# Optimization experiments

Hardware: AMD Instinct MI355X
Metric: run time of the kernel (lower is better)

Reference implementation:

```python
import jax, jax.numpy as jnp
import numpy as np

D = 768      # model dim
H = 12       # heads
HD = D // H  # head dim
FF = 3072    # mlp hidden = 4*D
EPS = 1e-5   # torch LayerNorm default eps


def setup_inputs() -> dict:
    key = jax.random.key(0)
    ks = jax.random.split(key, 8)
    init = lambda k, shp: (jax.random.normal(k, shp, jnp.float32) * 0.02)
    return {
        "x1": jax.random.normal(ks[0], (8, 512, D), jnp.float32),
        "x2": jax.random.normal(ks[1], (8, 1024, D), jnp.float32),
        "ln1_g": jnp.ones((D,), jnp.float32),
        "ln1_b": jnp.zeros((D,), jnp.float32),
        "w_qkv": init(ks[2], (D, 3 * D)),
        "b_qkv": jnp.zeros((3 * D,), jnp.float32),
        "w_proj": init(ks[3], (D, D)),
        "b_proj": jnp.zeros((D,), jnp.float32),
        "ls1": jnp.full((D,), 1e-5, jnp.float32),
        "ln2_g": jnp.ones((D,), jnp.float32),
        "ln2_b": jnp.zeros((D,), jnp.float32),
        "w_fc1": init(ks[4], (D, FF)),
        "b_fc1": jnp.zeros((FF,), jnp.float32),
        "w_fc2": init(ks[5], (FF, D)),
        "b_fc2": jnp.zeros((D,), jnp.float32),
        "ls2": jnp.full((D,), 1e-5, jnp.float32),
    }


def _ln(x, g, b):
    m = x.mean(-1, keepdims=True)
    v = ((x - m) ** 2).mean(-1, keepdims=True)
    return (x - m) * jax.lax.rsqrt(v + EPS) * g + b


def _block(x, ln1_g, ln1_b, w_qkv, b_qkv, w_proj, b_proj, ls1,
           ln2_g, ln2_b, w_fc1, b_fc1, w_fc2, b_fc2, ls2):
    # Block-diagonal attention over same-length group == independent per-sequence MHA.
    b, n, _ = x.shape
    h = _ln(x, ln1_g, ln1_b)
    qkv = h @ w_qkv + b_qkv                       # [b, n, 3D]
    q, k, v = [t.reshape(b, n, H, HD).transpose(0, 2, 1, 3)
               for t in jnp.split(qkv, 3, axis=-1)]
    scores = jnp.einsum('bhqd,bhkd->bhqk', q, k) * (HD ** -0.5)
    attn = jax.nn.softmax(scores, axis=-1)
    o = jnp.einsum('bhqk,bhkd->bhqd', attn, v).transpose(0, 2, 1, 3).reshape(b, n, D)
    x = x + ls1 * (o @ w_proj + b_proj)           # LayerScale + residual
    h2 = _ln(x, ln2_g, ln2_b)
    mlp = jax.nn.gelu(h2 @ w_fc1 + b_fc1, approximate=False) @ w_fc2 + b_fc2
    return x + ls2 * mlp


def reference(x1, x2, ln1_g, ln1_b, w_qkv, b_qkv, w_proj, b_proj, ls1,
              ln2_g, ln2_b, w_fc1, b_fc1, w_fc2, b_fc2, ls2):
    params = (ln1_g, ln1_b, w_qkv, b_qkv, w_proj, b_proj, ls1,
              ln2_g, ln2_b, w_fc1, b_fc1, w_fc2, b_fc2, ls2)
    y1 = _block(x1, *params)
    y2 = _block(x2, *params)
    # concatenated varlen token stream, equivalent to pre-split cat tensor
    return jnp.concatenate([y1.reshape(-1, D), y2.reshape(-1, D)], axis=0)
```

## Files before the change

### kernel.cpp

```cpp
#include <hip/hip_runtime.h>
#include <hip/hip_bf16.h>
#include <math.h>

typedef __hip_bfloat16 bf16_t;
typedef __bf16 bf16x8 __attribute__((ext_vector_type(8)));
typedef float f32x4 __attribute__((ext_vector_type(4)));
typedef float f32x16 __attribute__((ext_vector_type(16)));
typedef int int32x8 __attribute__((ext_vector_type(8)));
typedef int int4v __attribute__((ext_vector_type(4)));
typedef short short8v __attribute__((ext_vector_type(8)));

__device__ __forceinline__ void load_lds16(const void* g, void* l) {
    __builtin_amdgcn_global_load_lds(
        (__attribute__((address_space(1))) void*)g,
        (__attribute__((address_space(3))) void*)l, 16, 0, 0);
}

__device__ __forceinline__ unsigned char f32_fp8(float x) {
    return (unsigned char)(__builtin_amdgcn_cvt_pk_fp8_f32(x, 0.f, 0, false) & 0xff);
}

__global__ __launch_bounds__(256) void wconv_kernel(
    const float* __restrict__ W, unsigned char* __restrict__ Wt, int K, int N)
{
    __shared__ float tile[32][33];
    const int k0 = blockIdx.x * 32, n0 = blockIdx.y * 32;
    const int tx = threadIdx.x & 31, ty = threadIdx.x >> 5;
    #pragma unroll
    for (int i = 0; i < 32; i += 8)
        tile[ty + i][tx] = W[(size_t)(k0 + ty + i) * N + n0 + tx];
    __syncthreads();
    #pragma unroll
    for (int i = 0; i < 32; i += 8)
        Wt[(size_t)(n0 + ty + i) * K + k0 + tx] = f32_fp8(tile[tx][ty + i] * 64.f);
}

__global__ __launch_bounds__(256) void ln_kernel(
    const float* __restrict__ x0, const float* __restrict__ x1, int split,
    const float* __restrict__ g, const float* __restrict__ b,
    unsigned char* __restrict__ out)
{
    const int t = blockIdx.x;
    const int tid = threadIdx.x;
    const float* xr = (t < split) ? x0 + (size_t)t * 768
                                  : x1 + (size_t)(t - split) * 768;
    float v[3], s = 0.f, q = 0.f;
    #pragma unroll
    for (int i = 0; i < 3; ++i) {
        v[i] = xr[tid + i * 256];
        s += v[i]; q += v[i] * v[i];
    }
    #pragma unroll
    for (int o = 32; o > 0; o >>= 1) {
        s += __shfl_down(s, o);
        q += __shfl_down(q, o);
    }
    __shared__ float rs_[4], rq_[4];
    const int w = tid >> 6, lane = tid & 63;
    if (lane == 0) { rs_[w] = s; rq_[w] = q; }
    __syncthreads();
    s = rs_[0] + rs_[1] + rs_[2] + rs_[3];
    q = rq_[0] + rq_[1] + rq_[2] + rq_[3];
    const float mean = s * (1.f / 768.f);
    const float var  = q * (1.f / 768.f) - mean * mean;
    const float rstd = rsqrtf(var + 1e-5f);
    unsigned char* orow = out + (size_t)t * 768;
    #pragma unroll
    for (int i = 0; i < 3; ++i) {
        const int d = tid + i * 256;
        orow[d] = f32_fp8((v[i] - mean) * rstd * g[d] + b[d]);
    }
}

__device__ __forceinline__ int32x8 frag32(const unsigned char* S, int row, int lh) {
    const int rot = (row >> 1) & 3;
    const int t0 = lh * 2;
    const int4v lo = *(const int4v*)&S[row * 64 + (((t0 + rot) & 3) << 4)];
    const int4v hi = *(const int4v*)&S[row * 64 + (((t0 + 1 + rot) & 3) << 4)];
    int32x8 r;
    r[0] = lo[0]; r[1] = lo[1]; r[2] = lo[2]; r[3] = lo[3];
    r[4] = hi[0]; r[5] = hi[1]; r[6] = hi[2]; r[7] = hi[3];
    return r;
}

__global__ __launch_bounds__(256) void gemm_kernel(
    const unsigned char* __restrict__ A, const unsigned char* __restrict__ Bt,
    const float* __restrict__ bias, const float* __restrict__ ls,
    const float* __restrict__ resid0, const float* __restrict__ resid1, int rsplit,
    void* __restrict__ outp, bf16_t* __restrict__ vtout,
    int M, int N, int K, int mode)
{
    __shared__ __align__(16) unsigned char As[128 * 64];
    __shared__ __align__(16) unsigned char Bs[128 * 64];
    const int tid  = threadIdx.x;
    const int lane = tid & 63;
    const int w    = tid >> 6;
    const int wm   = w >> 1, wn = w & 1;
    const int l32  = lane & 31, lh = lane >> 5;
    const int bm   = blockIdx.x, bn = blockIdx.y;

    f32x16 acc[2][2];
    #pragma unroll
    for (int i = 0; i < 2; ++i)
        #pragma unroll
        for (int j = 0; j < 2; ++j)
            #pragma unroll
            for (int e = 0; e < 16; ++e) acc[i][j][e] = 0.f;

    const int srow   = lane >> 2;
    const int schunk = lane & 3;
    const unsigned char* Ag = A  + (size_t)(bm * 128) * K;
    const unsigned char* Bg = Bt + (size_t)(bn * 128) * K;

    for (int k0 = 0; k0 < K; k0 += 64) {
        #pragma unroll
        for (int p = 0; p < 2; ++p) {
            const int r = w * 32 + p * 16 + srow;
            const int gc = ((schunk - ((r >> 1) & 3)) & 3) * 16;
            load_lds16(Ag + (size_t)r * K + k0 + gc, &As[(w * 32 + p * 16) * 64]);
            load_lds16(Bg + (size_t)r * K + k0 + gc, &Bs[(w * 32 + p * 16) * 64]);
        }
        __syncthreads();
        int32x8 af[2], bf2[2];
        #pragma unroll
        for (int i = 0; i < 2; ++i)
            af[i] = frag32(As, wm * 64 + i * 32 + l32, lh);
        #pragma unroll
        for (int j = 0; j < 2; ++j)
            bf2[j] = frag32(Bs, wn * 64 + j * 32 + l32, lh);
        #pragma unroll
        for (int i = 0; i < 2; ++i)
            #pragma unroll
            for (int j = 0; j < 2; ++j)
                acc[i][j] = __builtin_amdgcn_mfma_scale_f32_32x32x64_f8f6f4(
                    af[i], bf2[j], acc[i][j], 0, 0,
                    0, 0x7F7F7F7F, 0, 0x7F7F7F7F);
        __syncthreads();
    }

    const float inv64 = 0.015625f;
    #pragma unroll
    for (int i = 0; i < 2; ++i) {
        #pragma unroll
        for (int j = 0; j < 2; ++j) {
            const int col  = bn * 128 + wn * 64 + j * 32 + l32;
            const int rowb = bm * 128 + wm * 64 + i * 32 + 4 * lh;
            const float bc = bias[col];
            if (mode == 3) {
                if (bn < 12) {
                    const float sc = (bn < 6) ? 0.125f : 1.f;
                    #pragma unroll
                    for (int g = 0; g < 4; ++g)
                        #pragma unroll
                        for (int r = 0; r < 4; ++r)
                            ((bf16_t*)outp)[(size_t)(rowb + 8 * g + r) * 1536 + col] =
                                __float2bfloat16((acc[i][j][4 * g + r] * inv64 + bc) * sc);
                } else {
                    #pragma unroll
                    for (int g = 0; g < 4; ++g) {
                        bf16_t tmp[4];
                        #pragma unroll
                        for (int r = 0; r < 4; ++r)
                            tmp[r] = __float2bfloat16(acc[i][j][4 * g + r] * inv64 + bc);
                        *(float2*)(vtout + (size_t)(col - 1536) * 12288 + rowb + 8 * g) =
                            *(const float2*)tmp;
                    }
                }
            } else if (mode == 1) {
                #pragma unroll
                for (int g = 0; g < 4; ++g)
                    #pragma unroll
                    for (int r = 0; r < 4; ++r) {
                        const float v = acc[i][j][4 * g + r] * inv64 + bc;
                        const float gl = v / (1.f + __expf(-1.702f * v));
                        ((unsigned char*)outp)[(size_t)(rowb + 8 * g + r) * N + col] =
                            f32_fp8(gl);
                    }
            } else {
                #pragma unroll
                for (int g = 0; g < 4; ++g)
                    #pragma unroll
                    for (int r = 0; r < 4; ++r) {
                        const int row = rowb + 8 * g + r;
                        const float v = acc[i][j][4 * g + r] * inv64 + bc;
                        const float rv = (row < rsplit)
                            ? resid0[(size_t)row * N + col]
                            : resid1[(size_t)(row - rsplit) * N + col];
                        ((float*)outp)[(size_t)row * N + col] = rv + ls[col] * v;
                    }
            }
        }
    }
}

__global__ __launch_bounds__(256) void attn_kernel(
    const bf16_t* __restrict__ qk, const bf16_t* __restrict__ vt,
    unsigned char* __restrict__ ao, int N, int tok_off)
{
    __shared__ __align__(16) bf16_t Qs[64 * 64];
    __shared__ __align__(16) bf16_t Kd[2][64 * 64];
    __shared__ __align__(16) bf16_t Vd[2][64 * 64];
    __shared__ __align__(16) bf16_t Ps[4 * 16 * 72];
    const int qt = blockIdx.x, h = blockIdx.y, s = blockIdx.z;
    const int tid = threadIdx.x, lane = tid & 63, w = tid >> 6;
    const int l4 = lane & 15, quad = lane >> 4;
    const int seq0 = tok_off + s * N;
    const int hoff = h * 64;
    const int lrow = lane >> 3;
    const int lcol = (((lane & 7) ^ (lrow & 7)) * 8);
    const int nkt = N >> 6;
    const int sw = l4 & 7;
    const int c0 = (quad ^ sw) * 8;
    const int c1 = ((quad + 4) ^ sw) * 8;

    #pragma unroll
    for (int p = 0; p < 2; ++p) {
        const int rr = w * 16 + p * 8;
        load_lds16(qk + (size_t)(seq0 + qt * 64 + rr + lrow) * 1536 + hoff + lcol,
                   &Qs[rr * 64]);
    }

    auto stageKV = [&](int kt, int buf) {
        #pragma unroll
        for (int p = 0; p < 2; ++p) {
            const int rr = w * 16 + p * 8;
            load_lds16(qk + (size_t)(seq0 + kt * 64 + rr + lrow) * 1536 + 768 + hoff + lcol,
                       &Kd[buf][rr * 64]);
            load_lds16(vt + (size_t)(hoff + rr + lrow) * 12288 + seq0 + kt * 64 + lcol,
                       &Vd[buf][rr * 64]);
        }
    };
    stageKV(0, 0);

    bf16x8 bones;
    {
        short8v t = {0x3F80, 0x3F80, 0x3F80, 0x3F80, 0x3F80, 0x3F80, 0x3F80, 0x3F80};
        __builtin_memcpy(&bones, &t, 16);
    }

    f32x4 oacc[4], lacc;
    #pragma unroll
    for (int j = 0; j < 4; ++j)
        #pragma unroll
        for (int e = 0; e < 4; ++e) oacc[j][e] = 0.f;
    #pragma unroll
    for (int e = 0; e < 4; ++e) lacc[e] = 0.f;

    bf16_t* Pw = &Ps[w * 16 * 72];

    for (int kt = 0; kt < nkt; ++kt) {
        const int buf = kt & 1;
        __syncthreads();
        if (kt + 1 < nkt) stageKV(kt + 1, buf ^ 1);

        f32x4 st[4];
        #pragma unroll
        for (int j = 0; j < 4; ++j)
            #pragma unroll
            for (int e = 0; e < 4; ++e) st[j][e] = 0.f;
        const bf16x8 aq0 = *(const bf16x8*)&Qs[(w * 16 + l4) * 64 + c0];
        const bf16x8 aq1 = *(const bf16x8*)&Qs[(w * 16 + l4) * 64 + c1];
        #pragma unroll
        for (int j = 0; j < 4; ++j) {
            const bf16x8 b0 = *(const bf16x8*)&Kd[buf][(j * 16 + l4) * 64 + c0];
            const bf16x8 b1 = *(const bf16x8*)&Kd[buf][(j * 16 + l4) * 64 + c1];
            st[j] = __builtin_amdgcn_mfma_f32_16x16x32_bf16(aq0, b0, st[j], 0, 0, 0);
            st[j] = __builtin_amdgcn_mfma_f32_16x16x32_bf16(aq1, b1, st[j], 0, 0, 0);
        }

        #pragma unroll
        for (int j = 0; j < 4; ++j)
            #pragma unroll
            for (int r = 0; r < 4; ++r)
                Pw[(quad * 4 + r) * 72 + j * 16 + l4] =
                    __float2bfloat16(__expf(st[j][r]));

        const bf16x8 ap0 = *(const bf16x8*)&Pw[l4 * 72 + quad * 8];
        const bf16x8 ap1 = *(const bf16x8*)&Pw[l4 * 72 + 32 + quad * 8];
        lacc = __builtin_amdgcn_mfma_f32_16x16x32_bf16(ap0, bones, lacc, 0, 0, 0);
        lacc = __builtin_amdgcn_mfma_f32_16x16x32_bf16(ap1, bones, lacc, 0, 0, 0);
        #pragma unroll
        for (int j = 0; j < 4; ++j) {
            const bf16x8 v0 = *(const bf16x8*)&Vd[buf][(j * 16 + l4) * 64 + c0];
            const bf16x8 v1 = *(const bf16x8*)&Vd[buf][(j * 16 + l4) * 64 + c1];
            oacc[j] = __builtin_amdgcn_mfma_f32_16x16x32_bf16(ap0, v0, oacc[j], 0, 0, 0);
            oacc[j] = __builtin_amdgcn_mfma_f32_16x16x32_bf16(ap1, v1, oacc[j], 0, 0, 0);
        }
    }

    unsigned char* Ps8 = (unsigned char*)Ps;
    #pragma unroll
    for (int r = 0; r < 4; ++r) {
        const float inv = 1.f / lacc[r];
        #pragma unroll
        for (int j = 0; j < 4; ++j)
            Ps8[(w * 16 + quad * 4 + r) * 64 + j * 16 + l4] =
                f32_fp8(oacc[j][r] * inv);
    }
    __syncthreads();
    #pragma unroll
    for (int p = 0; p < 2; ++p) {
        const int idx = p * 256 + tid;
        const int row = idx >> 3, j = idx & 7;
        *(unsigned long long*)(ao + (size_t)(seq0 + qt * 64 + row) * 768 + hoff + j * 8) =
            *(const unsigned long long*)&Ps8[row * 64 + j * 8];
    }
}

extern "C" void kernel_launch(void* const* d_in, const int* in_sizes, int n_in,
                              void* d_out, int out_size, void* d_ws, size_t ws_size,
                              hipStream_t stream)
{
    const float* x1     = (const float*)d_in[0];
    const float* x2     = (const float*)d_in[1];
    const float* ln1_g  = (const float*)d_in[2];
    const float* ln1_b  = (const float*)d_in[3];
    const float* w_qkv  = (const float*)d_in[4];
    const float* b_qkv  = (const float*)d_in[5];
    const float* w_proj = (const float*)d_in[6];
    const float* b_proj = (const float*)d_in[7];
    const float* ls1    = (const float*)d_in[8];
    const float* ln2_g  = (const float*)d_in[9];
    const float* ln2_b  = (const float*)d_in[10];
    const float* w_fc1  = (const float*)d_in[11];
    const float* b_fc1  = (const float*)d_in[12];
    const float* w_fc2  = (const float*)d_in[13];
    const float* b_fc2  = (const float*)d_in[14];
    const float* ls2    = (const float*)d_in[15];

    char* ws = (char*)d_ws;
    unsigned char* wqkv_t  = (unsigned char*)(ws + 0);
    unsigned char* wproj_t = (unsigned char*)(ws + 1769472);
    unsigned char* wfc1_t  = (unsigned char*)(ws + 2359296);
    unsigned char* wfc2_t  = (unsigned char*)(ws + 4718592);
    unsigned char* hbuf    = (unsigned char*)(ws + 7077888);
    bf16_t*        qkbuf   = (bf16_t*)(ws + 16515072);
    bf16_t*        vtbuf   = (bf16_t*)(ws + 54263808);
    unsigned char* hidbuf  = (unsigned char*)(ws + 16515072);
    unsigned char* aobuf   = (unsigned char*)(ws + 73138176);
    float*         xr      = (float*)(ws + 82575360);

    wconv_kernel<<<dim3(24, 72), 256, 0, stream>>>(w_qkv,  wqkv_t,  768, 2304);
    wconv_kernel<<<dim3(24, 24), 256, 0, stream>>>(w_proj, wproj_t, 768, 768);
    wconv_kernel<<<dim3(24, 96), 256, 0, stream>>>(w_fc1,  wfc1_t,  768, 3072);
    wconv_kernel<<<dim3(96, 24), 256, 0, stream>>>(w_fc2,  wfc2_t,  3072, 768);

    ln_kernel<<<12288, 256, 0, stream>>>(x1, x2, 4096, ln1_g, ln1_b, hbuf);

    gemm_kernel<<<dim3(96, 18), 256, 0, stream>>>(hbuf, wqkv_t, b_qkv, nullptr,
                                                  nullptr, nullptr, 0,
                                                  qkbuf, vtbuf, 12288, 2304, 768, 3);

    attn_kernel<<<dim3(8, 12, 8), 256, 0, stream>>>(qkbuf, vtbuf, aobuf, 512, 0);
    attn_kernel<<<dim3(16, 12, 8), 256, 0, stream>>>(qkbuf, vtbuf, aobuf, 1024, 4096);

    gemm_kernel<<<dim3(96, 6), 256, 0, stream>>>(aobuf, wproj_t, b_proj, ls1,
                                                 x1, x2, 4096,
                                                 xr, nullptr, 12288, 768, 768, 2);

    ln_kernel<<<12288, 256, 0, stream>>>(xr, xr, 1 << 30, ln2_g, ln2_b, hbuf);

    gemm_kernel<<<dim3(96, 24), 256, 0, stream>>>(hbuf, wfc1_t, b_fc1, nullptr,
                                                  nullptr, nullptr, 0,
                                                  hidbuf, nullptr, 12288, 3072, 768, 1);

    gemm_kernel<<<dim3(96, 6), 256, 0, stream>>>(hidbuf, wfc2_t, b_fc2, ls2,
                                                 xr, xr, 1 << 30,
                                                 (float*)d_out, nullptr, 12288, 768, 3072, 2);
}
```

Before: 417.5 us.

## Load GEMM MFMA fragments directly from global memory with register double-buffering

The FP8 GEMM no longer stages A and B tiles through LDS with block-wide barriers. Each wave loads its MFMA operand fragments straight from global memory into registers and prefetches the next K-tile while the current MFMAs run. This removes the LDS traffic and the __syncthreads per K step. In exchange, data shared between waves is fetched redundantly from global memory and L2, since each A row is now read by both wn waves and each B row by both wm waves. It also raises register pressure.

```diff
diff --git a/kernel.cpp b/kernel.cpp
--- a/kernel.cpp
+++ b/kernel.cpp
@@ -72,11 +72,9 @@
     }
 }
 
-__device__ __forceinline__ int32x8 frag32(const unsigned char* S, int row, int lh) {
-    const int rot = (row >> 1) & 3;
-    const int t0 = lh * 2;
-    const int4v lo = *(const int4v*)&S[row * 64 + (((t0 + rot) & 3) << 4)];
-    const int4v hi = *(const int4v*)&S[row * 64 + (((t0 + 1 + rot) & 3) << 4)];
+__device__ __forceinline__ int32x8 fragG(const unsigned char* g) {
+    const int4v lo = *(const int4v*)g;
+    const int4v hi = *(const int4v*)(g + 16);
     int32x8 r;
     r[0] = lo[0]; r[1] = lo[1]; r[2] = lo[2]; r[3] = lo[3];
     r[4] = hi[0]; r[5] = hi[1]; r[6] = hi[2]; r[7] = hi[3];
@@ -90,8 +88,6 @@
     void* __restrict__ outp, bf16_t* __restrict__ vtout,
     int M, int N, int K, int mode)
 {
-    __shared__ __align__(16) unsigned char As[128 * 64];
-    __shared__ __align__(16) unsigned char Bs[128 * 64];
     const int tid  = threadIdx.x;
     const int lane = tid & 63;
     const int w    = tid >> 6;
@@ -107,35 +103,35 @@
             #pragma unroll
             for (int e = 0; e < 16; ++e) acc[i][j][e] = 0.f;
 
-    const int srow   = lane >> 2;
-    const int schunk = lane & 3;
-    const unsigned char* Ag = A  + (size_t)(bm * 128) * K;
-    const unsigned char* Bg = Bt + (size_t)(bn * 128) * K;
-
-    for (int k0 = 0; k0 < K; k0 += 64) {
-        #pragma unroll
-        for (int p = 0; p < 2; ++p) {
-            const int r = w * 32 + p * 16 + srow;
-            const int gc = ((schunk - ((r >> 1) & 3)) & 3) * 16;
-            load_lds16(Ag + (size_t)r * K + k0 + gc, &As[(w * 32 + p * 16) * 64]);
-            load_lds16(Bg + (size_t)r * K + k0 + gc, &Bs[(w * 32 + p * 16) * 64]);
-        }
-        __syncthreads();
-        int32x8 af[2], bf2[2];
-        #pragma unroll
-        for (int i = 0; i < 2; ++i)
-            af[i] = frag32(As, wm * 64 + i * 32 + l32, lh);
-        #pragma unroll
-        for (int j = 0; j < 2; ++j)
-            bf2[j] = frag32(Bs, wn * 64 + j * 32 + l32, lh);
+    const unsigned char* ap[2];
+    const unsigned char* bp[2];
+    #pragma unroll
+    for (int i = 0; i < 2; ++i)
+        ap[i] = A + (size_t)(bm * 128 + wm * 64 + i * 32 + l32) * K + lh * 32;
+    #pragma unroll
+    for (int j = 0; j < 2; ++j)
+        bp[j] = Bt + (size_t)(bn * 128 + wn * 64 + j * 32 + l32) * K + lh * 32;
+
+    int32x8 ca[2], cb[2], na[2], nb[2];
+    #pragma unroll
+    for (int i = 0; i < 2; ++i) { ca[i] = fragG(ap[i]); cb[i] = fragG(bp[i]); }
+
+    const int nk = K >> 6;
+    for (int kt = 0; kt < nk; ++kt) {
+        if (kt + 1 < nk) {
+            const int kn = (kt + 1) << 6;
+            #pragma unroll
+            for (int i = 0; i < 2; ++i) { na[i] = fragG(ap[i] + kn); nb[i] = fragG(bp[i] + kn); }
+        }
         #pragma unroll
         for (int i = 0; i < 2; ++i)
             #pragma unroll
             for (int j = 0; j < 2; ++j)
                 acc[i][j] = __builtin_amdgcn_mfma_scale_f32_32x32x64_f8f6f4(
-                    af[i], bf2[j], acc[i][j], 0, 0,
+                    ca[i], cb[j], acc[i][j], 0, 0,
                     0, 0x7F7F7F7F, 0, 0x7F7F7F7F);
-        __syncthreads();
+        #pragma unroll
+        for (int i = 0; i < 2; ++i) { ca[i] = na[i]; cb[i] = nb[i]; }
     }
 
     const float inv64 = 0.015625f;
```

After: 623.8 us. 1.49x slower.
